# Kernel tuning notes

Measured on AMD Instinct MI355X. Metric: run time of the kernel, lower is better.

The kernel has to match this reference:

```python
import jax, jax.numpy as jnp
import numpy as np

B, S, D, H, R, N, RK = 2, 2048, 1024, 16, 64, 32, 128
DH = D // H
EPS = 1e-5


def setup_inputs() -> dict:
    key = jax.random.key(0)
    ks = jax.random.split(key, 24)
    f = lambda i, shape, sc=1.0: jax.random.normal(ks[i], shape, dtype=jnp.float32) * sc
    sm = lambda i, shape: jax.nn.softmax(f(i, shape), axis=-1)
    return {
        'x': f(0, (B, S, D)),
        'f_qk': f(1, (N, D, R), 0.02), 'f_v': f(2, (N, D, R), 0.02),
        'r_qk': f(3, (N, R, D), 0.02), 'r_v': f(4, (N, R, D), 0.02),
        'f_know': f(5, (N, D, RK), 0.02), 'r_know': f(6, (N, RK, D), 0.02),
        'W_O': f(7, (D, D), 0.02),
        'gamma1': jnp.ones(D, jnp.float32), 'beta1': jnp.zeros(D, jnp.float32),
        'gamma2': jnp.ones(D, jnp.float32), 'beta2': jnp.zeros(D, jnp.float32),
        'w_fq': sm(8, (B, S, N)), 'w_fk': sm(9, (B, S, N)), 'w_fv': sm(10, (B, S, N)),
        'w_rq': sm(11, (B, S, N)), 'w_rk': sm(12, (B, S, N)), 'w_rv': sm(13, (B, S, N)),
        'w_know_f': sm(14, (B, S, N)), 'w_know_r': sm(15, (B, S, N)),
    }


def _ln(x, g, b):
    mu = jnp.mean(x, axis=-1, keepdims=True)
    var = jnp.mean(jnp.square(x - mu), axis=-1, keepdims=True)
    return g * (x - mu) * jax.lax.rsqrt(var + EPS) + b


def _feature(x, neurons, w):
    # x [B,S,D], neurons [N,D,R], w [B,S,N] -> [B,S,R]
    all_h = jnp.einsum('bsd,ndr->bsnr', x, neurons)
    return jnp.einsum('bsnr,bsn->bsr', all_h, w)


def _restore(h, neurons, w):
    # h [B,S,R], neurons [N,R,D], w [B,S,N] -> [B,S,D]
    # fuse: avoid materializing [B,S,N,D]; outer-product [B,S,N,R] is small
    t = w[..., None] * h[:, :, None, :]
    return jnp.einsum('bsnr,nrd->bsd', t, neurons)


def _causal_attn(Q, K, V):
    # Q,K,V: [B,H,S,DH]
    scale = 1.0 / jnp.sqrt(jnp.asarray(DH, Q.dtype))
    scores = jnp.einsum('bhqd,bhkd->bhqk', Q, K) * scale
    mask = jnp.tril(jnp.ones((S, S), bool))
    scores = jnp.where(mask, scores, jnp.asarray(-jnp.inf, scores.dtype))
    probs = jax.nn.softmax(scores, axis=-1)
    return jnp.einsum('bhqk,bhkd->bhqd', probs, V)


def reference(x, f_qk, f_v, r_qk, r_v, f_know, r_know, W_O,
              gamma1, beta1, gamma2, beta2,
              w_fq, w_fk, w_fv, w_rq, w_rk, w_rv, w_know_f, w_know_r):
    # --- attention circuit ---
    nx = _ln(x, gamma1, beta1)
    h_q = _feature(nx, f_qk, w_fq)
    h_k = _feature(nx, f_qk, w_fk)
    h_v = _feature(nx, f_v, w_fv)
    Q = _restore(h_q, r_qk, w_rq)
    K = _restore(h_k, r_qk, w_rk)
    V = _restore(h_v, r_v, w_rv)
    to_heads = lambda t: t.reshape(B, S, H, DH).transpose(0, 2, 1, 3)
    attn = _causal_attn(to_heads(Q), to_heads(K), to_heads(V))
    attn = attn.transpose(0, 2, 1, 3).reshape(B, S, D)
    attn_out = attn @ W_O.T  # nn.Linear(d_model, d_model, bias=False)
    x = x + attn_out
    # --- knowledge circuit ---
    nx2 = _ln(x, gamma2, beta2)
    h = _feature(nx2, f_know, w_know_f)
    know_out = _restore(h, r_know, w_know_r)
    x = x + know_out
    return x
```

## Files before the change

kernel.cpp:

```cpp
#include <hip/hip_runtime.h>
#include <stdint.h>


typedef __bf16 bf16x8 __attribute__((ext_vector_type(8)));
typedef float f32x4 __attribute__((ext_vector_type(4)));

__device__ __forceinline__ unsigned short f2b(float f) {
  union { float f; unsigned u; } v; v.f = f;
  unsigned u = v.u;
  unsigned r = (u + 0x7FFFu + ((u >> 16) & 1u)) >> 16;
  return (unsigned short)r;
}
__device__ __forceinline__ float b2f(unsigned short h) {
  union { unsigned u; float f; } v; v.u = ((unsigned)h) << 16;
  return v.f;
}
__device__ __forceinline__ unsigned pk2(float lo, float hi) {
  return (unsigned)f2b(lo) | ((unsigned)f2b(hi) << 16);
}
__device__ __forceinline__ unsigned pkt(float lo, float hi) {
  union { float f; unsigned u; } a, b; a.f = lo; b.f = hi;
  return __builtin_amdgcn_perm(b.u, a.u, 0x07060302u);
}
__device__ __forceinline__ f32x4 vmax4(f32x4 a, f32x4 b) {
  f32x4 r;
  r[0] = fmaxf(a[0], b[0]); r[1] = fmaxf(a[1], b[1]);
  r[2] = fmaxf(a[2], b[2]); r[3] = fmaxf(a[3], b[3]);
  return r;
}

__global__ __launch_bounds__(256, 3) void gemm_bt(
    const unsigned short* __restrict__ A, const unsigned short* __restrict__ Bt,
    void* __restrict__ out, int K) {
  __shared__ unsigned short lsA[128 * 64];
  __shared__ unsigned short lsB[128 * 64];
  const int N = 4096;
  const int bid = blockIdx.x;
  const int xcd = bid & 7, j = bid >> 3;
  const int row0 = (xcd * 4 + (j >> 5)) * 128;
  const int col0 = (j & 31) * 128;
  const int tid = threadIdx.x;
  const int w = tid >> 6, lane = tid & 63;
  const int quad = lane >> 4, l16 = lane & 15;
  const int wr = w >> 1, wc = w & 1;

  const int srow = w * 32 + (lane >> 3);
  const int scg = ((lane & 7) ^ (lane >> 3)) * 8;
  const unsigned short* ap = A + (size_t)(row0 + srow) * K + scg;
  const unsigned short* bp = Bt + (size_t)(col0 + srow) * K + scg;

  const f32x4 fz = {0.f, 0.f, 0.f, 0.f};
  f32x4 acc[4][4];
#pragma unroll
  for (int i = 0; i < 4; ++i)
#pragma unroll
    for (int jj = 0; jj < 4; ++jj) acc[i][jj] = fz;

  for (int k0 = 0; k0 < K; k0 += 64) {
#pragma unroll
    for (int i = 0; i < 4; ++i) {
      __builtin_amdgcn_global_load_lds(
          (const __attribute__((address_space(1))) unsigned int*)(ap + (size_t)i * 8 * K + k0),
          (__attribute__((address_space(3))) unsigned int*)&lsA[(w * 32 + i * 8) * 64],
          16, 0, 0);
      __builtin_amdgcn_global_load_lds(
          (const __attribute__((address_space(1))) unsigned int*)(bp + (size_t)i * 8 * K + k0),
          (__attribute__((address_space(3))) unsigned int*)&lsB[(w * 32 + i * 8) * 64],
          16, 0, 0);
    }
    __syncthreads();
#pragma unroll
    for (int kk = 0; kk < 2; ++kk) {
      bf16x8 af[4], bfr[4];
      const int sl = (((kk * 4 + quad) ^ (l16 & 7)) * 8);
#pragma unroll
      for (int mt = 0; mt < 4; ++mt)
        af[mt] = *(const bf16x8*)&lsA[(wr * 64 + mt * 16 + l16) * 64 + sl];
#pragma unroll
      for (int nt = 0; nt < 4; ++nt)
        bfr[nt] = *(const bf16x8*)&lsB[(wc * 64 + nt * 16 + l16) * 64 + sl];
#pragma unroll
      for (int mt = 0; mt < 4; ++mt)
#pragma unroll
        for (int nt = 0; nt < 4; ++nt)
          acc[mt][nt] = __builtin_amdgcn_mfma_f32_16x16x32_bf16(af[mt], bfr[nt], acc[mt][nt], 0, 0, 0);
    }
    __syncthreads();
  }

  const int rb = row0 + wr * 64;
  const int cb = col0 + wc * 64;
#pragma unroll
  for (int mt = 0; mt < 4; ++mt) {
#pragma unroll
    for (int nt = 0; nt < 4; ++nt) {
      const int r = rb + mt * 16 + quad * 4;
      const int c = cb + nt * 16 + l16;
#pragma unroll
      for (int i = 0; i < 4; ++i)
        ((unsigned short*)out)[(size_t)(r + i) * N + c] = f2b(acc[mt][nt][i]);
    }
  }
}

__global__ __launch_bounds__(256, 3) void gemm_qkv(
    const unsigned short* __restrict__ t_qk, const unsigned short* __restrict__ t_v,
    const unsigned short* __restrict__ r_qkT, const unsigned short* __restrict__ r_vT,
    unsigned short* __restrict__ QK, unsigned short* __restrict__ VT) {
  __shared__ unsigned short lsA[128 * 64];
  __shared__ unsigned short lsB[128 * 64];
  const int K = 2048;
  const int bid = blockIdx.x;
  const unsigned short* A;
  const unsigned short* Bt;
  int row0, col0, isv;
  if (bid < 256) {
    const int xcd = bid & 7, j = bid >> 3;
    row0 = (xcd * 4 + (j >> 3)) * 128;
    col0 = (j & 7) * 128;
    A = t_v; Bt = r_vT; isv = 1;
  } else {
    const int u = bid - 256;
    const int xcd = u & 7, j = u >> 3;
    row0 = (xcd * 8 + (j >> 3)) * 128;
    col0 = (j & 7) * 128;
    A = t_qk; Bt = r_qkT; isv = 0;
  }
  const int tid = threadIdx.x;
  const int w = tid >> 6, lane = tid & 63;
  const int quad = lane >> 4, l16 = lane & 15;
  const int wr = w >> 1, wc = w & 1;

  const int srow = w * 32 + (lane >> 3);
  const int scg = ((lane & 7) ^ (lane >> 3)) * 8;
  const unsigned short* ap = A + (size_t)(row0 + srow) * K + scg;
  const unsigned short* bp = Bt + (size_t)(col0 + srow) * K + scg;

  const f32x4 fz = {0.f, 0.f, 0.f, 0.f};
  f32x4 acc[4][4];
#pragma unroll
  for (int i = 0; i < 4; ++i)
#pragma unroll
    for (int jj = 0; jj < 4; ++jj) acc[i][jj] = fz;

  for (int k0 = 0; k0 < K; k0 += 64) {
#pragma unroll
    for (int i = 0; i < 4; ++i) {
      __builtin_amdgcn_global_load_lds(
          (const __attribute__((address_space(1))) unsigned int*)(ap + (size_t)i * 8 * K + k0),
          (__attribute__((address_space(3))) unsigned int*)&lsA[(w * 32 + i * 8) * 64],
          16, 0, 0);
      __builtin_amdgcn_global_load_lds(
          (const __attribute__((address_space(1))) unsigned int*)(bp + (size_t)i * 8 * K + k0),
          (__attribute__((address_space(3))) unsigned int*)&lsB[(w * 32 + i * 8) * 64],
          16, 0, 0);
    }
    __syncthreads();
#pragma unroll
    for (int kk = 0; kk < 2; ++kk) {
      bf16x8 af[4], bfr[4];
      const int sl = (((kk * 4 + quad) ^ (l16 & 7)) * 8);
#pragma unroll
      for (int mt = 0; mt < 4; ++mt)
        af[mt] = *(const bf16x8*)&lsA[(wr * 64 + mt * 16 + l16) * 64 + sl];
#pragma unroll
      for (int nt = 0; nt < 4; ++nt)
        bfr[nt] = *(const bf16x8*)&lsB[(wc * 64 + nt * 16 + l16) * 64 + sl];
#pragma unroll
      for (int mt = 0; mt < 4; ++mt)
#pragma unroll
        for (int nt = 0; nt < 4; ++nt)
          acc[mt][nt] = __builtin_amdgcn_mfma_f32_16x16x32_bf16(af[mt], bfr[nt], acc[mt][nt], 0, 0, 0);
    }
    __syncthreads();
  }

  const int rb = row0 + wr * 64;
  const int cb = col0 + wc * 64;
#pragma unroll
  for (int mt = 0; mt < 4; ++mt) {
#pragma unroll
    for (int nt = 0; nt < 4; ++nt) {
      const int r = rb + mt * 16 + quad * 4;
      const int c = cb + nt * 16 + l16;
#pragma unroll
      for (int i = 0; i < 4; ++i) {
        const float v = acc[mt][nt][i];
        if (isv) VT[(size_t)c * 4096 + (r + i)] = f2b(v);
        else QK[(size_t)(r + i) * 1024 + c] = f2b(v);
      }
    }
  }
}

__global__ __launch_bounds__(256, 3) void gemm_ks4(
    const unsigned short* __restrict__ A, const unsigned short* __restrict__ Bt,
    float* __restrict__ p0, float* __restrict__ p1,
    float* __restrict__ p2, float* __restrict__ p3, int K) {
  __shared__ unsigned short lsA[128 * 64];
  __shared__ unsigned short lsB[128 * 64];
  const int N = 1024;
  const int bid = blockIdx.x;
  const int xcd = bid & 7, j = bid >> 3;
  const int row_l = j >> 5, rem = j & 31;
  const int ks = rem >> 3, col = rem & 7;
  const int row0 = (xcd * 4 + row_l) * 128;
  const int col0 = col * 128;
  const int kq = K >> 2;
  const int kbeg = ks * kq, kend = kbeg + kq;
  const int tid = threadIdx.x;
  const int w = tid >> 6, lane = tid & 63;
  const int quad = lane >> 4, l16 = lane & 15;
  const int wr = w >> 1, wc = w & 1;

  const int srow = w * 32 + (lane >> 3);
  const int scg = ((lane & 7) ^ (lane >> 3)) * 8;
  const unsigned short* ap = A + (size_t)(row0 + srow) * K + scg;
  const unsigned short* bp = Bt + (size_t)(col0 + srow) * K + scg;

  const f32x4 fz = {0.f, 0.f, 0.f, 0.f};
  f32x4 acc[4][4];
#pragma unroll
  for (int i = 0; i < 4; ++i)
#pragma unroll
    for (int jj = 0; jj < 4; ++jj) acc[i][jj] = fz;

  for (int k0 = kbeg; k0 < kend; k0 += 64) {
#pragma unroll
    for (int i = 0; i < 4; ++i) {
      __builtin_amdgcn_global_load_lds(
          (const __attribute__((address_space(1))) unsigned int*)(ap + (size_t)i * 8 * K + k0),
          (__attribute__((address_space(3))) unsigned int*)&lsA[(w * 32 + i * 8) * 64],
          16, 0, 0);
      __builtin_amdgcn_global_load_lds(
          (const __attribute__((address_space(1))) unsigned int*)(bp + (size_t)i * 8 * K + k0),
          (__attribute__((address_space(3))) unsigned int*)&lsB[(w * 32 + i * 8) * 64],
          16, 0, 0);
    }
    __syncthreads();
#pragma unroll
    for (int kk = 0; kk < 2; ++kk) {
      bf16x8 af[4], bfr[4];
      const int sl = (((kk * 4 + quad) ^ (l16 & 7)) * 8);
#pragma unroll
      for (int mt = 0; mt < 4; ++mt)
        af[mt] = *(const bf16x8*)&lsA[(wr * 64 + mt * 16 + l16) * 64 + sl];
#pragma unroll
      for (int nt = 0; nt < 4; ++nt)
        bfr[nt] = *(const bf16x8*)&lsB[(wc * 64 + nt * 16 + l16) * 64 + sl];
#pragma unroll
      for (int mt = 0; mt < 4; ++mt)
#pragma unroll
        for (int nt = 0; nt < 4; ++nt)
          acc[mt][nt] = __builtin_amdgcn_mfma_f32_16x16x32_bf16(af[mt], bfr[nt], acc[mt][nt], 0, 0, 0);
    }
    __syncthreads();
  }

  float* out = (ks == 0) ? p0 : (ks == 1) ? p1 : (ks == 2) ? p2 : p3;
  const int rb = row0 + wr * 64;
  const int cb = col0 + wc * 64;
#pragma unroll
  for (int mt = 0; mt < 4; ++mt) {
#pragma unroll
    for (int nt = 0; nt < 4; ++nt) {
      const int r = rb + mt * 16 + quad * 4;
      const int c = cb + nt * 16 + l16;
#pragma unroll
      for (int i = 0; i < 4; ++i)
        out[(size_t)(r + i) * N + c] = acc[mt][nt][i];
    }
  }
}

__global__ __launch_bounds__(256) void gemm_wo_res(
    const unsigned short* __restrict__ A, const unsigned short* __restrict__ Bt,
    const float* __restrict__ res, float* __restrict__ out) {
  __shared__ unsigned short lsA[128 * 64];
  __shared__ unsigned short lsB[64 * 64];
  const int K = 1024, N = 1024;
  const int bid = blockIdx.x;
  const int xcd = bid & 7, j = bid >> 3;
  const int row0 = (xcd * 4 + (j & 3)) * 128;
  const int col0 = (j >> 2) * 64;
  const int tid = threadIdx.x;
  const int w = tid >> 6, lane = tid & 63;
  const int quad = lane >> 4, l16 = lane & 15;
  const int wr = w >> 1, wc = w & 1;

  const int srowA = w * 32 + (lane >> 3);
  const int srowB = w * 16 + (lane >> 3);
  const int scg = ((lane & 7) ^ (lane >> 3)) * 8;
  const unsigned short* ap = A + (size_t)(row0 + srowA) * K + scg;
  const unsigned short* bp = Bt + (size_t)(col0 + srowB) * K + scg;

  const f32x4 fz = {0.f, 0.f, 0.f, 0.f};
  f32x4 acc[4][2];
#pragma unroll
  for (int i = 0; i < 4; ++i)
#pragma unroll
    for (int jj = 0; jj < 2; ++jj) acc[i][jj] = fz;

  for (int k0 = 0; k0 < K; k0 += 64) {
#pragma unroll
    for (int i = 0; i < 4; ++i)
      __builtin_amdgcn_global_load_lds(
          (const __attribute__((address_space(1))) unsigned int*)(ap + (size_t)i * 8 * K + k0),
          (__attribute__((address_space(3))) unsigned int*)&lsA[(w * 32 + i * 8) * 64],
          16, 0, 0);
#pragma unroll
    for (int i = 0; i < 2; ++i)
      __builtin_amdgcn_global_load_lds(
          (const __attribute__((address_space(1))) unsigned int*)(bp + (size_t)i * 8 * K + k0),
          (__attribute__((address_space(3))) unsigned int*)&lsB[(w * 16 + i * 8) * 64],
          16, 0, 0);
    __syncthreads();
#pragma unroll
    for (int kk = 0; kk < 2; ++kk) {
      bf16x8 af[4], bfr[2];
      const int sl = (((kk * 4 + quad) ^ (l16 & 7)) * 8);
#pragma unroll
      for (int mt = 0; mt < 4; ++mt)
        af[mt] = *(const bf16x8*)&lsA[(wr * 64 + mt * 16 + l16) * 64 + sl];
#pragma unroll
      for (int nt = 0; nt < 2; ++nt)
        bfr[nt] = *(const bf16x8*)&lsB[(wc * 32 + nt * 16 + l16) * 64 + sl];
#pragma unroll
      for (int mt = 0; mt < 4; ++mt)
#pragma unroll
        for (int nt = 0; nt < 2; ++nt)
          acc[mt][nt] = __builtin_amdgcn_mfma_f32_16x16x32_bf16(af[mt], bfr[nt], acc[mt][nt], 0, 0, 0);
    }
    __syncthreads();
  }

  const int rb = row0 + wr * 64;
  const int cb = col0 + wc * 32;
#pragma unroll
  for (int mt = 0; mt < 4; ++mt) {
#pragma unroll
    for (int nt = 0; nt < 2; ++nt) {
      const int r = rb + mt * 16 + quad * 4;
      const int c = cb + nt * 16 + l16;
#pragma unroll
      for (int i = 0; i < 4; ++i)
        out[(size_t)(r + i) * N + c] = acc[mt][nt][i] + res[(size_t)(r + i) * N + c];
    }
  }
}

__global__ __launch_bounds__(256) void reduce_add5(
    const float* __restrict__ p0, const float* __restrict__ p1,
    const float* __restrict__ p2, const float* __restrict__ p3,
    const float* __restrict__ res, float* __restrict__ out) {
  const int i = (blockIdx.x * 256 + threadIdx.x) * 4;
  const f32x4 a = *(const f32x4*)&p0[i];
  const f32x4 b = *(const f32x4*)&p1[i];
  const f32x4 c = *(const f32x4*)&p2[i];
  const f32x4 d = *(const f32x4*)&p3[i];
  const f32x4 e = *(const f32x4*)&res[i];
  f32x4 o;
#pragma unroll
  for (int k = 0; k < 4; ++k) o[k] = ((a[k] + b[k]) + (c[k] + d[k])) + e[k];
  *(f32x4*)&out[i] = o;
}

__global__ __launch_bounds__(256) void ln_kernel(
    const float* __restrict__ x, const float* __restrict__ g,
    const float* __restrict__ be, unsigned short* __restrict__ out) {
  __shared__ float sbuf[4];
  const int t = blockIdx.x, tid = threadIdx.x;
  const float* row = x + (size_t)t * 1024;
  float v[4], s = 0.f;
#pragma unroll
  for (int j = 0; j < 4; ++j) { v[j] = row[tid + j * 256]; s += v[j]; }
#pragma unroll
  for (int off = 32; off; off >>= 1) s += __shfl_xor(s, off);
  if ((tid & 63) == 0) sbuf[tid >> 6] = s;
  __syncthreads();
  const float mu = (sbuf[0] + sbuf[1] + sbuf[2] + sbuf[3]) * (1.f / 1024.f);
  __syncthreads();
  float ss = 0.f;
#pragma unroll
  for (int j = 0; j < 4; ++j) { const float d = v[j] - mu; ss += d * d; }
#pragma unroll
  for (int off = 32; off; off >>= 1) ss += __shfl_xor(ss, off);
  if ((tid & 63) == 0) sbuf[tid >> 6] = ss;
  __syncthreads();
  const float var = (sbuf[0] + sbuf[1] + sbuf[2] + sbuf[3]) * (1.f / 1024.f);
  const float rstd = rsqrtf(var + 1e-5f);
  unsigned short* orow = out + (size_t)t * 1024;
#pragma unroll
  for (int j = 0; j < 4; ++j) {
    const int c = tid + j * 256;
    orow[c] = f2b((v[j] - mu) * rstd * g[c] + be[c]);
  }
}

__global__ __launch_bounds__(256) void mix_attn(
    const unsigned short* __restrict__ all_h,
    const float* __restrict__ w_fq, const float* __restrict__ w_fk,
    const float* __restrict__ w_fv, const float* __restrict__ w_rq,
    const float* __restrict__ w_rk, const float* __restrict__ w_rv,
    unsigned short* __restrict__ t_qk, unsigned short* __restrict__ t_v) {
  __shared__ float hq[64], hk[64], hv[64];
  const int t = blockIdx.x, tid = threadIdx.x;
  const int wvi = tid >> 6, lane = tid & 63;
  const unsigned short* row = all_h + (size_t)t * 4096;
  if (wvi < 3) {
    const float* wf = (wvi == 0 ? w_fq : wvi == 1 ? w_fk : w_fv) + (size_t)t * 32;
    const int base = (wvi == 2) ? 2048 : 0;
    float acc = 0.f;
#pragma unroll
    for (int n = 0; n < 32; ++n) acc += wf[n] * b2f(row[base + n * 64 + lane]);
    (wvi == 0 ? hq : wvi == 1 ? hk : hv)[lane] = acc;
  }
  __syncthreads();
  const int n = tid >> 3, r0 = (tid & 7) * 8;
  const float wq = w_rq[(size_t)t * 32 + n];
  const float wk = w_rk[(size_t)t * 32 + n];
  const float wv2 = w_rv[(size_t)t * 32 + n];
  unsigned dq[4], dk[4], dv[4];
#pragma unroll
  for (int jj = 0; jj < 4; ++jj) {
    dq[jj] = pk2(wq * hq[r0 + 2 * jj], wq * hq[r0 + 2 * jj + 1]);
    dk[jj] = pk2(wk * hk[r0 + 2 * jj], wk * hk[r0 + 2 * jj + 1]);
    dv[jj] = pk2(wv2 * hv[r0 + 2 * jj], wv2 * hv[r0 + 2 * jj + 1]);
  }
  *(uint4*)&t_qk[(size_t)t * 2048 + tid * 8] = *(uint4*)dq;
  *(uint4*)&t_qk[(size_t)(4096 + t) * 2048 + tid * 8] = *(uint4*)dk;
  *(uint4*)&t_v[(size_t)t * 2048 + tid * 8] = *(uint4*)dv;
}

__global__ __launch_bounds__(256) void mix_know(
    const unsigned short* __restrict__ all_h, const float* __restrict__ w_f,
    const float* __restrict__ w_r, unsigned short* __restrict__ t_know) {
  __shared__ float h[128];
  const int t = blockIdx.x, tid = threadIdx.x;
  const unsigned short* row = all_h + (size_t)t * 4096;
  if (tid < 128) {
    const float* wf = w_f + (size_t)t * 32;
    float acc = 0.f;
#pragma unroll
    for (int n = 0; n < 32; ++n) acc += wf[n] * b2f(row[n * 128 + tid]);
    h[tid] = acc;
  }
  __syncthreads();
  const int n = tid >> 3, r0 = (tid & 7) * 16;
  const float wn = w_r[(size_t)t * 32 + n];
  unsigned d[8];
#pragma unroll
  for (int jj = 0; jj < 8; ++jj)
    d[jj] = pk2(wn * h[r0 + 2 * jj], wn * h[r0 + 2 * jj + 1]);
  *(uint4*)&t_know[(size_t)t * 4096 + tid * 16] = *(uint4*)d;
  *(uint4*)&t_know[(size_t)t * 4096 + tid * 16 + 8] = *(uint4*)&d[4];
}

__global__ __launch_bounds__(256) void prep_all(
    const float* __restrict__ f_qk, const float* __restrict__ f_v,
    const float* __restrict__ f_know, const float* __restrict__ r_qk,
    const float* __restrict__ r_v, const float* __restrict__ r_know,
    const float* __restrict__ W_O,
    unsigned short* __restrict__ fcomb, unsigned short* __restrict__ fknowT,
    unsigned short* __restrict__ r_qkT, unsigned short* __restrict__ r_vT,
    unsigned short* __restrict__ r_knowT, unsigned short* __restrict__ WO_bf) {
  __shared__ float tile[32][33];
  const int bid = blockIdx.x;
  const int tx = threadIdx.x, ty = threadIdx.y;
  const float* in;
  unsigned short* out;
  int R, C, gx, loc;
  if (bid < 2048)       { in = f_qk;   out = fcomb;                         R = 1024; C = 64;   gx = 2;  loc = bid; }
  else if (bid < 4096)  { in = f_v;    out = fcomb + (size_t)2048 * 1024;   R = 1024; C = 64;   gx = 2;  loc = bid - 2048; }
  else if (bid < 8192)  { in = f_know; out = fknowT;                        R = 1024; C = 128;  gx = 4;  loc = bid - 4096; }
  else if (bid < 10240) { in = r_qk;   out = r_qkT;                         R = 2048; C = 1024; gx = 32; loc = bid - 8192; }
  else if (bid < 12288) { in = r_v;    out = r_vT;                          R = 2048; C = 1024; gx = 32; loc = bid - 10240; }
  else if (bid < 16384) { in = r_know; out = r_knowT;                       R = 4096; C = 1024; gx = 32; loc = bid - 12288; }
  else {
    const int i = ((bid - 16384) * 256 + ty * 32 + tx) * 4;
    const f32x4 v = *(const f32x4*)&W_O[i];
    *(unsigned*)&WO_bf[i] = pk2(v[0], v[1]);
    *(unsigned*)&WO_bf[i + 2] = pk2(v[2], v[3]);
    return;
  }
  const int tiles = gx * (R >> 5);
  const int bb = loc / tiles, rem = loc % tiles;
  const int r0 = (rem / gx) * 32, c0 = (rem % gx) * 32;
  const float* ip = in + (size_t)bb * R * C;
  unsigned short* op = out + (size_t)bb * R * C;
#pragma unroll
  for (int j = 0; j < 4; ++j)
    tile[ty + j * 8][tx] = ip[(size_t)(r0 + ty + j * 8) * C + c0 + tx];
  __syncthreads();
#pragma unroll
  for (int j = 0; j < 4; ++j)
    op[(size_t)(c0 + ty + j * 8) * R + r0 + tx] = f2b(tile[tx][ty + j * 8]);
}

__global__ __launch_bounds__(256) void flash_split(
    const unsigned short* __restrict__ Q, const unsigned short* __restrict__ Kp,
    const unsigned short* __restrict__ VT, unsigned short* __restrict__ O,
    float* __restrict__ Opart, float* __restrict__ ml) {
  __shared__ unsigned short Kls[2][64 * 64];
  __shared__ unsigned short Vls[2][64 * 64];
  const int uidx = 79 - (int)blockIdx.x;
  int uu = uidx, qt = 0, ch = 0;
  for (int q = 0; q < 32; ++q) {
    const int n = (q >> 3) + 1;
    if (uu < n) { qt = q; ch = uu; break; }
    uu -= n;
  }
  const int bh = blockIdx.y;
  const int b = bh >> 4, h = bh & 15;
  const int tid = threadIdx.x;
  const int w = tid >> 6, lane = tid & 63, quad = lane >> 4, l16 = lane & 15;
  const int tb = b * 2048;
  const int qrow = qt * 64 + w * 16;
  const int ktlo = ch * 8;
  const int kthi = min(qt, ch * 8 + 7);
  const float C = 0.18033688f;

  const int srow = (lane >> 3);
  const int scol = ((lane & 7) ^ srow) * 8;

  bf16x8 qf[2];
#pragma unroll
  for (int kk = 0; kk < 2; ++kk)
    qf[kk] = *(const bf16x8*)&Q[(size_t)(tb + qrow + l16) * 1024 + h * 64 + kk * 32 + quad * 8];

  const f32x4 fz = {0.f, 0.f, 0.f, 0.f};
  float m_i = -1e30f, l_i = 0.f;
  f32x4 o_acc[4];
#pragma unroll
  for (int nt = 0; nt < 4; ++nt) o_acc[nt] = fz;

  auto stage = [&](int buf, int kt) {
#pragma unroll
    for (int j = 0; j < 2; ++j) {
      const int rg = (w * 2 + j) * 8 + srow;
      __builtin_amdgcn_global_load_lds(
          (const __attribute__((address_space(1))) unsigned int*)
              (Kp + (size_t)(tb + kt * 64 + rg) * 1024 + h * 64 + scol),
          (__attribute__((address_space(3))) unsigned int*)&Kls[buf][(w * 2 + j) * 8 * 64],
          16, 0, 0);
      __builtin_amdgcn_global_load_lds(
          (const __attribute__((address_space(1))) unsigned int*)
              (VT + (size_t)(h * 64 + rg) * 4096 + tb + kt * 64 + scol),
          (__attribute__((address_space(3))) unsigned int*)&Vls[buf][(w * 2 + j) * 8 * 64],
          16, 0, 0);
    }
  };

  const int srcA = (((quad & 1) * 32 + l16) << 2);
  const int srcB = srcA + 64;
  const bool hiq = (quad >= 2);

  auto pv_block = [&](f32x4* s, bf16x8* vf, const f32x4& rsv) {
    unsigned pk[4][2];
#pragma unroll
    for (int nt = 0; nt < 4; ++nt) {
      pk[nt][0] = pkt(s[nt][0], s[nt][1]);
      pk[nt][1] = pkt(s[nt][2], s[nt][3]);
    }
#pragma unroll
    for (int kk = 0; kk < 2; ++kk) {
      const int ea = 2 * kk, eb = 2 * kk + 1;
      const unsigned u0 = __builtin_amdgcn_ds_bpermute(srcA, pk[ea][0]);
      const unsigned u1 = __builtin_amdgcn_ds_bpermute(srcA, pk[ea][1]);
      const unsigned u2 = __builtin_amdgcn_ds_bpermute(srcB, pk[ea][0]);
      const unsigned u3 = __builtin_amdgcn_ds_bpermute(srcB, pk[ea][1]);
      const unsigned w0 = __builtin_amdgcn_ds_bpermute(srcA, pk[eb][0]);
      const unsigned w1 = __builtin_amdgcn_ds_bpermute(srcA, pk[eb][1]);
      const unsigned w2 = __builtin_amdgcn_ds_bpermute(srcB, pk[eb][0]);
      const unsigned w3 = __builtin_amdgcn_ds_bpermute(srcB, pk[eb][1]);
      unsigned dw[4];
      dw[0] = hiq ? w0 : u0;
      dw[1] = hiq ? w1 : u1;
      dw[2] = hiq ? w2 : u2;
      dw[3] = hiq ? w3 : u3;
      const bf16x8 pf = *(const bf16x8*)dw;
      __builtin_amdgcn_s_setprio(1);
#pragma unroll
      for (int nt = 0; nt < 4; ++nt)
        o_acc[nt] = __builtin_amdgcn_mfma_f32_16x16x32_bf16(vf[kk * 4 + nt], pf, o_acc[nt], 0, 0, 0);
      __builtin_amdgcn_s_setprio(0);
    }
    float rs = (rsv[0] + rsv[1]) + (rsv[2] + rsv[3]);
    rs += __shfl_xor(rs, 16);
    rs += __shfl_xor(rs, 32);
    l_i += rs;
  };

  stage(0, ktlo);
  __syncthreads();
  int buf = 0;

  const bool hasdiag = (ch == (qt >> 3));
  const int ktnd = hasdiag ? kthi - 1 : kthi;

  for (int kt = ktlo; kt <= ktnd; ++kt) {
    if (kt < kthi) stage(buf ^ 1, kt + 1);
    bf16x8 kf[8], vf[8];
#pragma unroll
    for (int kk = 0; kk < 2; ++kk)
#pragma unroll
      for (int nt = 0; nt < 4; ++nt) {
        const int sl = (((kk * 4 + quad) ^ (l16 & 7)) * 8);
        kf[kk * 4 + nt] = *(const bf16x8*)&Kls[buf][(nt * 16 + l16) * 64 + sl];
        vf[kk * 4 + nt] = *(const bf16x8*)&Vls[buf][(nt * 16 + l16) * 64 + sl];
      }

    f32x4 s[4];
    __builtin_amdgcn_s_setprio(1);
#pragma unroll
    for (int nt = 0; nt < 4; ++nt)
      s[nt] = __builtin_amdgcn_mfma_f32_16x16x32_bf16(kf[nt], qf[0], fz, 0, 0, 0);
#pragma unroll
    for (int nt = 0; nt < 4; ++nt)
      s[nt] = __builtin_amdgcn_mfma_f32_16x16x32_bf16(kf[4 + nt], qf[1], s[nt], 0, 0, 0);
    __builtin_amdgcn_s_setprio(0);

    const f32x4 m4 = vmax4(vmax4(s[0], s[1]), vmax4(s[2], s[3]));
    float mx = fmaxf(fmaxf(m4[0], m4[1]), fmaxf(m4[2], m4[3]));
    mx = fmaxf(mx, __shfl_xor(mx, 16));
    mx = fmaxf(mx, __shfl_xor(mx, 32));
    if (!__all(mx <= m_i)) {
      const float mn = fmaxf(m_i, mx);
      const float al = exp2f((m_i - mn) * C);
      m_i = mn;
      l_i *= al;
#pragma unroll
      for (int nt = 0; nt < 4; ++nt) o_acc[nt] *= al;
    }
    const float mC = m_i * C;
    f32x4 rsv = fz;
#pragma unroll
    for (int nt = 0; nt < 4; ++nt) {
      f32x4 e = s[nt] * C - mC;
      f32x4 p;
#pragma unroll
      for (int i = 0; i < 4; ++i) p[i] = exp2f(e[i]);
      s[nt] = p;
      rsv += p;
    }
    pv_block(s, vf, rsv);
    __syncthreads();
    buf ^= 1;
  }

  if (hasdiag) {
    bf16x8 kf[8], vf[8];
#pragma unroll
    for (int kk = 0; kk < 2; ++kk)
#pragma unroll
      for (int nt = 0; nt < 4; ++nt) {
        const int sl = (((kk * 4 + quad) ^ (l16 & 7)) * 8);
        kf[kk * 4 + nt] = *(const bf16x8*)&Kls[buf][(nt * 16 + l16) * 64 + sl];
        vf[kk * 4 + nt] = *(const bf16x8*)&Vls[buf][(nt * 16 + l16) * 64 + sl];
      }
    const int ntmax = w + 1;
    f32x4 s[4];
#pragma unroll
    for (int nt = 0; nt < 4; ++nt) s[nt] = fz;
    __builtin_amdgcn_s_setprio(1);
#pragma unroll
    for (int kk = 0; kk < 2; ++kk)
#pragma unroll
      for (int nt = 0; nt < 4; ++nt)
        if (nt < ntmax)
          s[nt] = __builtin_amdgcn_mfma_f32_16x16x32_bf16(kf[kk * 4 + nt], qf[kk], s[nt], 0, 0, 0);
    __builtin_amdgcn_s_setprio(0);

    const int qloc = w * 16 + l16;
    float mxs[4] = {-1e30f, -1e30f, -1e30f, -1e30f};
#pragma unroll
    for (int nt = 0; nt < 4; ++nt) {
      if (nt >= ntmax) continue;
#pragma unroll
      for (int i = 0; i < 4; ++i) {
        float v = s[nt][i];
        if ((nt * 16 + quad * 4 + i) > qloc) v = -1e30f;
        s[nt][i] = v;
        mxs[nt] = fmaxf(mxs[nt], v);
      }
    }
    float mx = fmaxf(fmaxf(mxs[0], mxs[1]), fmaxf(mxs[2], mxs[3]));
    mx = fmaxf(mx, __shfl_xor(mx, 16));
    mx = fmaxf(mx, __shfl_xor(mx, 32));
    if (!__all(mx <= m_i)) {
      const float mn = fmaxf(m_i, mx);
      const float al = exp2f((m_i - mn) * C);
      m_i = mn;
      l_i *= al;
#pragma unroll
      for (int nt = 0; nt < 4; ++nt) o_acc[nt] *= al;
    }
    const float mC = m_i * C;
    f32x4 rsv = fz;
#pragma unroll
    for (int nt = 0; nt < 4; ++nt) {
      if (nt >= ntmax) { s[nt] = fz; continue; }
      f32x4 e = s[nt] * C - mC;
      f32x4 p;
#pragma unroll
      for (int i = 0; i < 4; ++i) p[i] = exp2f(e[i]);
      s[nt] = p;
      rsv += p;
    }
    pv_block(s, vf, rsv);
  }

  const int nch = (qt >> 3) + 1;
  if (nch == 1) {
    const float inv = 1.0f / l_i;
    unsigned short* orow = O + (size_t)(tb + qrow + l16) * 1024 + h * 64;
#pragma unroll
    for (int nt = 0; nt < 4; ++nt) {
      const unsigned d0 = pk2(o_acc[nt][0] * inv, o_acc[nt][1] * inv);
      const unsigned d1 = pk2(o_acc[nt][2] * inv, o_acc[nt][3] * inv);
      *(unsigned*)&orow[nt * 16 + quad * 4] = d0;
      *(unsigned*)&orow[nt * 16 + quad * 4 + 2] = d1;
    }
  } else {
    const int slot = bh * 80 + uidx;
    const int lq = w * 16 + l16;
    float* op = Opart + ((size_t)slot * 64 + lq) * 64;
#pragma unroll
    for (int nt = 0; nt < 4; ++nt)
      *(f32x4*)&op[nt * 16 + quad * 4] = o_acc[nt];
    if (quad == 0) {
      ml[(size_t)slot * 128 + lq * 2] = m_i;
      ml[(size_t)slot * 128 + lq * 2 + 1] = l_i;
    }
  }
}

__global__ __launch_bounds__(256) void flash_reduce(
    const float* __restrict__ Opart, const float* __restrict__ ml,
    unsigned short* __restrict__ O) {
  const int qt = 8 + blockIdx.x;
  const int bh = blockIdx.y;
  const int b = bh >> 4, h = bh & 15;
  const int j = qt >> 3;
  const int base = 8 * (j * (j + 1) / 2) + (qt - 8 * j) * (j + 1);
  const int nch = j + 1;
  const int tid = threadIdx.x;
  const int lq = tid >> 2, dq = (tid & 3) * 16;
  const float C = 0.18033688f;

  float mc[4], lc[4];
  float m = -1e30f;
#pragma unroll
  for (int c = 0; c < 4; ++c) {
    if (c < nch) {
      const size_t sl = (size_t)(bh * 80 + base + c) * 128 + lq * 2;
      mc[c] = ml[sl];
      lc[c] = ml[sl + 1];
    } else { mc[c] = -1e30f; lc[c] = 0.f; }
    m = fmaxf(m, mc[c]);
  }
  float fac[4], lt = 0.f;
#pragma unroll
  for (int c = 0; c < 4; ++c) {
    fac[c] = (c < nch) ? exp2f((mc[c] - m) * C) : 0.f;
    lt += fac[c] * lc[c];
  }
  const float inv = 1.0f / lt;
  float acc[16];
#pragma unroll
  for (int i = 0; i < 16; ++i) acc[i] = 0.f;
#pragma unroll
  for (int c = 0; c < 4; ++c) {
    if (c >= nch) continue;
    const float* op = Opart + ((size_t)(bh * 80 + base + c) * 64 + lq) * 64 + dq;
#pragma unroll
    for (int i = 0; i < 16; i += 4) {
      const f32x4 v = *(const f32x4*)&op[i];
#pragma unroll
      for (int k = 0; k < 4; ++k) acc[i + k] += fac[c] * v[k];
    }
  }
  unsigned short* orow = O + (size_t)(b * 2048 + qt * 64 + lq) * 1024 + h * 64 + dq;
#pragma unroll
  for (int i = 0; i < 16; i += 2)
    *(unsigned*)&orow[i] = pk2(acc[i] * inv, acc[i + 1] * inv);
}

extern "C" void kernel_launch(void* const* d_in, const int* in_sizes, int n_in,
                              void* d_out, int out_size, void* d_ws, size_t ws_size,
                              hipStream_t stream) {
  (void)in_sizes; (void)n_in; (void)out_size; (void)ws_size;
  const float* x      = (const float*)d_in[0];
  const float* f_qk   = (const float*)d_in[1];
  const float* f_v    = (const float*)d_in[2];
  const float* r_qk   = (const float*)d_in[3];
  const float* r_v    = (const float*)d_in[4];
  const float* f_know = (const float*)d_in[5];
  const float* r_know = (const float*)d_in[6];
  const float* W_O    = (const float*)d_in[7];
  const float* gamma1 = (const float*)d_in[8];
  const float* beta1  = (const float*)d_in[9];
  const float* gamma2 = (const float*)d_in[10];
  const float* beta2  = (const float*)d_in[11];
  const float* w_fq   = (const float*)d_in[12];
  const float* w_fk   = (const float*)d_in[13];
  const float* w_fv   = (const float*)d_in[14];
  const float* w_rq   = (const float*)d_in[15];
  const float* w_rk   = (const float*)d_in[16];
  const float* w_rv   = (const float*)d_in[17];
  const float* w_kf   = (const float*)d_in[18];
  const float* w_kr   = (const float*)d_in[19];

  char* base = (char*)d_ws;
  size_t off = 0;
  auto alloc = [&](size_t b) { char* p = base + off; off += (b + 255) & ~(size_t)255; return p; };
  unsigned short* fcomb   = (unsigned short*)alloc(8388608);
  unsigned short* fknowT  = (unsigned short*)alloc(8388608);
  unsigned short* r_qkT   = (unsigned short*)alloc(4194304);
  unsigned short* r_vT    = (unsigned short*)alloc(4194304);
  unsigned short* r_knowT = (unsigned short*)alloc(8388608);
  unsigned short* WO_bf   = (unsigned short*)alloc(2097152);
  unsigned short* nx_bf   = (unsigned short*)alloc(8388608);
  unsigned short* all_h   = (unsigned short*)alloc(33554432);
  unsigned short* t_qk    = (unsigned short*)alloc(33554432);
  unsigned short* t_v     = (unsigned short*)alloc(16777216);
  unsigned short* QKbuf   = (unsigned short*)alloc(16777216);
  unsigned short* VT      = (unsigned short*)alloc(8388608);
  unsigned short* attn    = (unsigned short*)alloc(8388608);
  float* x1 = (float*)t_v;
  float* Opart = (float*)all_h;
  float* mlbuf = (float*)((char*)all_h + 41943040);
  float* pW0 = (float*)all_h;
  float* pW1 = (float*)((char*)all_h + 16777216);
  float* pW2 = (float*)QKbuf;
  float* pW3_know = (float*)VT;

  const dim3 blk256(256), blkT(32, 8);

  prep_all<<<17408, blkT, 0, stream>>>(f_qk, f_v, f_know, r_qk, r_v, r_know, W_O,
                                       fcomb, fknowT, r_qkT, r_vT, r_knowT, WO_bf);

  ln_kernel<<<4096, blk256, 0, stream>>>(x, gamma1, beta1, nx_bf);
  gemm_bt<<<1024, blk256, 0, stream>>>(nx_bf, fcomb, all_h, 1024);
  mix_attn<<<4096, blk256, 0, stream>>>(all_h, w_fq, w_fk, w_fv, w_rq, w_rk, w_rv, t_qk, t_v);
  gemm_qkv<<<768, blk256, 0, stream>>>(t_qk, t_v, r_qkT, r_vT, QKbuf, VT);
  flash_split<<<dim3(80, 32), blk256, 0, stream>>>(QKbuf, QKbuf + (size_t)4096 * 1024, VT, attn,
                                                   Opart, mlbuf);
  flash_reduce<<<dim3(24, 32), blk256, 0, stream>>>(Opart, mlbuf, attn);
  gemm_wo_res<<<512, blk256, 0, stream>>>(attn, WO_bf, x, x1);

  ln_kernel<<<4096, blk256, 0, stream>>>(x1, gamma2, beta2, nx_bf);
  gemm_bt<<<1024, blk256, 0, stream>>>(nx_bf, fknowT, all_h, 1024);
  mix_know<<<4096, blk256, 0, stream>>>(all_h, w_kf, w_kr, t_qk);
  gemm_ks4<<<1024, blk256, 0, stream>>>(t_qk, r_knowT, pW0, pW1, pW2, pW3_know, 4096);
  reduce_add5<<<4096, blk256, 0, stream>>>(pW0, pW1, pW2, pW3_know, x1, (float*)d_out);
}
```

Baseline: 493.4 us.

## Load K/V fragments directly from global memory in flash attention, dropping LDS staging

Removes the double-buffered LDS staging of K and V tiles (global_load_lds plus __syncthreads). Each wave now reads its MFMA fragments straight from global memory through per-lane pointers that advance every key tile, and the launch bounds now request 3 blocks per CU. This removes the LDS traffic and block-wide barriers. In exchange, each of the 4 waves re-fetches the same K/V from global/L2, and the prefetch overlap from the next-tile staging is lost, so latency may be exposed.

```diff
diff --git a/kernel.cpp b/kernel.cpp
--- a/kernel.cpp
+++ b/kernel.cpp
@@ -497,12 +497,10 @@
     op[(size_t)(c0 + ty + j * 8) * R + r0 + tx] = f2b(tile[tx][ty + j * 8]);
 }
 
-__global__ __launch_bounds__(256) void flash_split(
+__global__ __launch_bounds__(256, 3) void flash_split(
     const unsigned short* __restrict__ Q, const unsigned short* __restrict__ Kp,
     const unsigned short* __restrict__ VT, unsigned short* __restrict__ O,
     float* __restrict__ Opart, float* __restrict__ ml) {
-  __shared__ unsigned short Kls[2][64 * 64];
-  __shared__ unsigned short Vls[2][64 * 64];
   const int uidx = 79 - (int)blockIdx.x;
   int uu = uidx, qt = 0, ch = 0;
   for (int q = 0; q < 32; ++q) {
@@ -520,9 +518,6 @@
   const int kthi = min(qt, ch * 8 + 7);
   const float C = 0.18033688f;
 
-  const int srow = (lane >> 3);
-  const int scol = ((lane & 7) ^ srow) * 8;
-
   bf16x8 qf[2];
 #pragma unroll
   for (int kk = 0; kk < 2; ++kk)
@@ -534,22 +529,13 @@
 #pragma unroll
   for (int nt = 0; nt < 4; ++nt) o_acc[nt] = fz;
 
-  auto stage = [&](int buf, int kt) {
-#pragma unroll
-    for (int j = 0; j < 2; ++j) {
-      const int rg = (w * 2 + j) * 8 + srow;
-      __builtin_amdgcn_global_load_lds(
-          (const __attribute__((address_space(1))) unsigned int*)
-              (Kp + (size_t)(tb + kt * 64 + rg) * 1024 + h * 64 + scol),
-          (__attribute__((address_space(3))) unsigned int*)&Kls[buf][(w * 2 + j) * 8 * 64],
-          16, 0, 0);
-      __builtin_amdgcn_global_load_lds(
-          (const __attribute__((address_space(1))) unsigned int*)
-              (VT + (size_t)(h * 64 + rg) * 4096 + tb + kt * 64 + scol),
-          (__attribute__((address_space(3))) unsigned int*)&Vls[buf][(w * 2 + j) * 8 * 64],
-          16, 0, 0);
-    }
-  };
+  const unsigned short* kb[4];
+  const unsigned short* vb[4];
+#pragma unroll
+  for (int nt = 0; nt < 4; ++nt) {
+    kb[nt] = Kp + (size_t)(tb + ktlo * 64 + nt * 16 + l16) * 1024 + h * 64 + quad * 8;
+    vb[nt] = VT + (size_t)(h * 64 + nt * 16 + l16) * 4096 + tb + ktlo * 64 + quad * 8;
+  }
 
   const int srcA = (((quad & 1) * 32 + l16) << 2);
   const int srcB = srcA + 64;
@@ -591,24 +577,23 @@
     l_i += rs;
   };
 
-  stage(0, ktlo);
-  __syncthreads();
-  int buf = 0;
-
   const bool hasdiag = (ch == (qt >> 3));
   const int ktnd = hasdiag ? kthi - 1 : kthi;
 
   for (int kt = ktlo; kt <= ktnd; ++kt) {
-    if (kt < kthi) stage(buf ^ 1, kt + 1);
     bf16x8 kf[8], vf[8];
 #pragma unroll
-    for (int kk = 0; kk < 2; ++kk)
-#pragma unroll
-      for (int nt = 0; nt < 4; ++nt) {
-        const int sl = (((kk * 4 + quad) ^ (l16 & 7)) * 8);
-        kf[kk * 4 + nt] = *(const bf16x8*)&Kls[buf][(nt * 16 + l16) * 64 + sl];
-        vf[kk * 4 + nt] = *(const bf16x8*)&Vls[buf][(nt * 16 + l16) * 64 + sl];
-      }
+    for (int nt = 0; nt < 4; ++nt) {
+      kf[nt]     = *(const bf16x8*)(kb[nt]);
+      kf[4 + nt] = *(const bf16x8*)(kb[nt] + 32);
+    }
+#pragma unroll
+    for (int nt = 0; nt < 4; ++nt) {
+      vf[nt]     = *(const bf16x8*)(vb[nt]);
+      vf[4 + nt] = *(const bf16x8*)(vb[nt] + 32);
+    }
+#pragma unroll
+    for (int nt = 0; nt < 4; ++nt) { kb[nt] += 64 * 1024; vb[nt] += 64; }
 
     f32x4 s[4];
     __builtin_amdgcn_s_setprio(1);
@@ -644,20 +629,17 @@
       rsv += p;
     }
     pv_block(s, vf, rsv);
-    __syncthreads();
-    buf ^= 1;
   }
 
   if (hasdiag) {
     bf16x8 kf[8], vf[8];
 #pragma unroll
-    for (int kk = 0; kk < 2; ++kk)
-#pragma unroll
-      for (int nt = 0; nt < 4; ++nt) {
-        const int sl = (((kk * 4 + quad) ^ (l16 & 7)) * 8);
-        kf[kk * 4 + nt] = *(const bf16x8*)&Kls[buf][(nt * 16 + l16) * 64 + sl];
-        vf[kk * 4 + nt] = *(const bf16x8*)&Vls[buf][(nt * 16 + l16) * 64 + sl];
-      }
+    for (int nt = 0; nt < 4; ++nt) {
+      kf[nt]     = *(const bf16x8*)(kb[nt]);
+      kf[4 + nt] = *(const bf16x8*)(kb[nt] + 32);
+      vf[nt]     = *(const bf16x8*)(vb[nt]);
+      vf[4 + nt] = *(const bf16x8*)(vb[nt] + 32);
+    }
     const int ntmax = w + 1;
     f32x4 s[4];
 #pragma unroll
```

Measured after the change: 575.1 us. 16.6% more time.
